# Performance work log

Measured on AMD Instinct MI355X. Metric: run time of the kernel, lower is better.

## Reference

```python
import jax, jax.numpy as jnp
import numpy as np

N = 50000   # nodes
E = 800000  # edges per timestep
T = 2
IN_C = 128
HID = 128


def gcn_conv(x, src, dst, W, b):
    """PyG GCNConv: add self-loops, symmetric normalization, linear, scatter-add, bias."""
    n = x.shape[0]
    loop = jnp.arange(n, dtype=src.dtype)
    s = jnp.concatenate([src, loop])  # [E+N]
    d = jnp.concatenate([dst, loop])
    h = x @ W                          # [N, H]
    deg = jax.ops.segment_sum(jnp.ones_like(d, dtype=x.dtype), d, num_segments=n)
    dinv = jnp.where(deg > 0, jax.lax.rsqrt(deg), 0.0)
    norm = dinv[s] * dinv[d]           # [E+N]
    msg = h[s] * norm[:, None]         # gather + scale
    out = jax.ops.segment_sum(msg, d, num_segments=n)  # scatter-add
    return out + b


def setup_inputs() -> dict:
    key = jax.random.key(0)
    ks = jax.random.split(key, 6)
    x_seq = jax.random.normal(ks[0], (T, N, IN_C), dtype=jnp.float32)
    edge_indices = jax.random.randint(ks[1], (T, 2, E), 0, N, dtype=jnp.int64)
    W1 = jax.random.normal(ks[2], (IN_C, HID), dtype=jnp.float32) * (1.0 / np.sqrt(IN_C))
    b1 = jnp.zeros((HID,), dtype=jnp.float32)
    W2 = jax.random.normal(ks[3], (HID, HID), dtype=jnp.float32) * (1.0 / np.sqrt(HID))
    b2 = jnp.zeros((HID,), dtype=jnp.float32)
    Wc = jax.random.normal(ks[4], (HID, 1), dtype=jnp.float32) * (1.0 / np.sqrt(HID))
    bc = jnp.zeros((1,), dtype=jnp.float32)
    return {"x_seq": x_seq, "edge_indices": edge_indices, "W1": W1, "b1": b1,
            "W2": W2, "b2": b2, "Wc": Wc, "bc": bc}


def reference(x_seq, edge_indices, W1, b1, W2, b2, Wc, bc):
    outputs = []
    for t in range(T):  # small fixed timestep loop, as in original
        x_t = x_seq[t]
        src = edge_indices[t, 0]
        dst = edge_indices[t, 1]
        h = jax.nn.relu(gcn_conv(x_t, src, dst, W1, b1))
        # dropout is inference-identity (eval mode)
        h = gcn_conv(h, src, dst, W2, b2)
        outputs.append(h)
    final = outputs[-1]
    importance_out = (final @ Wc + bc).squeeze(-1)  # [N]
    return (importance_out, *outputs)
```

## Files before the change

kernel.cpp:

```cpp
#include <hip/hip_runtime.h>
#include <hip/hip_bf16.h>

typedef unsigned int u32;
typedef unsigned short u16;
typedef unsigned long long u64;
typedef __bf16 bf16x8 __attribute__((ext_vector_type(8)));
typedef short short8 __attribute__((ext_vector_type(8)));
typedef float floatx4 __attribute__((ext_vector_type(4)));

__device__ inline float b2f(u16 b) { return __uint_as_float((u32)b << 16); }
__device__ inline float lo2f(u32 p) { return __uint_as_float(p << 16); }
__device__ inline float hi2f(u32 p) { return __uint_as_float(p & 0xffff0000u); }
__device__ inline u16 f2bs(float f) {
    __hip_bfloat16 h = __float2bfloat16(f);
    return *reinterpret_cast<u16*>(&h);
}
__device__ inline float ldext(const void* p, int fl, int i) {
    return fl ? ((const float*)p)[i] : b2f(((const u16*)p)[i]);
}

__global__ __launch_bounds__(64) void detect_kernel(const int* __restrict__ eb,
                                                    const u32* __restrict__ xw,
                                                    int* __restrict__ flags,
                                                    int* __restrict__ bkcnt,
                                                    int* __restrict__ ovfcur,
                                                    int S, int n) {
    __shared__ int sh[64 * 3];
    int lane = threadIdx.x & 63;
    for (int j = lane; j < 512; j += 64) bkcnt[j] = 0;
    if (lane == 0) *ovfcur = 0;
    int zc = 0, explo = 0;
#pragma unroll
    for (int r = 0; r < 4; ++r) {
        int i = 64 * r + lane;
        zc += (eb[2 * i + 1] == 0) ? 1 : 0;
        u32 w = xw[i];
        int e = (int)((w >> 7) & 0xFF);
        explo += (e >= 96 && e <= 140) ? 1 : 0;
    }
    sh[lane] = zc;
    sh[64 + lane] = explo;
    __syncthreads();
    int fl = 0;
    {
        int z = 0;
        for (int j = 0; j < 64; ++j) z += sh[j];
        fl = (z > 200) ? 1 : 0;
    }
    int vc = 0;
#pragma unroll
    for (int r = 0; r < 4; ++r) {
        int li = S / 2 + 64 * r + lane;
        int v = fl ? eb[2 * li] : eb[li];
        vc += ((unsigned)v < (unsigned)n) ? 1 : 0;
    }
    sh[128 + lane] = vc;
    __syncthreads();
    if (lane == 0) {
        int vtot = 0, etot = 0;
        for (int j = 0; j < 64; ++j) vtot += sh[128 + j];
        for (int j = 0; j < 64; ++j) etot += sh[64 + j];
        flags[0] = fl;
        flags[1] = (etot >= 192) ? 0 : 1;
        flags[2] = (vtot >= 240) ? (S / 4) : (S / 8);
    }
}

__device__ inline int load_edge(const int* eb, int fl, int idx) {
    return eb[fl ? (idx << 1) : idx];
}

#define PCHUNK 4096
__global__ __launch_bounds__(256) void part_kernel(const int* __restrict__ eb,
                                                   const int* __restrict__ flags,
                                                   int* __restrict__ bkcnt,
                                                   u64* __restrict__ pairs,
                                                   int n, int shift, int capP,
                                                   int gP,
                                                   const void* __restrict__ W1,
                                                   const void* __restrict__ W2,
                                                   u16* __restrict__ W1t,
                                                   u16* __restrict__ W2t) {
    __shared__ int cnt[512];
    __shared__ int gbase[512];
    if ((int)blockIdx.x >= gP) {
        int tid = (blockIdx.x - gP) * 256 + threadIdx.x;
        if (tid < 2 * 128 * 128) {
            int which = tid >> 14;
            int r = tid & 16383;
            const void* W = which ? W2 : W1;
            u16* Wt = which ? W2t : W1t;
            int c = r >> 7, k = r & 127;
            Wt[c * 128 + k] = f2bs(ldext(W, flags[1], k * 128 + c));
        }
        return;
    }
    const int E = flags[2];
    const int fl = flags[0];
    const int nbuk = (2 * n + (1 << shift) - 1) >> shift;
    const int tid = threadIdx.x;
    for (int i = tid; i < nbuk; i += 256) cnt[i] = 0;
    __syncthreads();
    const int e0 = blockIdx.x * PCHUNK;
    u32 sv[16]; int gv[16], rk[16];
#pragma unroll
    for (int j = 0; j < 16; ++j) {
        int e = e0 + j * 256 + tid;
        u32 gs = 0; int g = -1;
        if (e < 2 * E) {
            int t = (e >= E) ? 1 : 0;
            int le = e - t * E;
            gs = (u32)(t * n) + (u32)load_edge(eb, fl, t * 2 * E + le);
            unsigned du = (unsigned)load_edge(eb, fl, t * 2 * E + E + le);
            if (du < (unsigned)n) g = t * n + (int)du;
        }
        sv[j] = gs;
        gv[j] = g;
        rk[j] = (g >= 0) ? atomicAdd(&cnt[g >> shift], 1) : 0;
    }
    __syncthreads();
    for (int b = tid; b < nbuk; b += 256) {
        int c = cnt[b];
        gbase[b] = c ? atomicAdd(&bkcnt[b], c) : 0;
    }
    __syncthreads();
#pragma unroll
    for (int j = 0; j < 16; ++j) {
        if (gv[j] >= 0) {
            int b = gv[j] >> shift;
            int idx = gbase[b] + rk[j];
            if (idx < capP)
                pairs[(size_t)b * capP + idx] =
                    ((u64)(u32)gv[j] << 32) | sv[j];
        }
    }
}

__global__ __launch_bounds__(256) void scat_kernel(const u64* __restrict__ pairs,
                                                   const int* __restrict__ bkcnt,
                                                   int* __restrict__ deg,
                                                   float* __restrict__ dinv,
                                                   int* __restrict__ ssrc,
                                                   int* __restrict__ ovf,
                                                   int* __restrict__ ovfoff,
                                                   int* __restrict__ ovfcur,
                                                   int n2, int shift, int capP) {
    __shared__ int hist[1024];
    __shared__ int cur[1024];
    const int b = blockIdx.x;
    const int d0 = b << shift;
    if (d0 >= n2) return;
    int nn = (1 << shift);
    if (d0 + nn > n2) nn = n2 - d0;
    const int tid = threadIdx.x;
    for (int j = tid; j < nn; j += 256) { hist[j] = 0; cur[j] = 0; }
    __syncthreads();
    int cnt = bkcnt[b];
    if (cnt > capP) cnt = capP;
    const u64* pb = pairs + (size_t)b * capP;
    for (int i = tid; i < cnt; i += 256) {
        unsigned dl = (unsigned)(int)(pb[i] >> 32) - (unsigned)d0;
        if (dl < (unsigned)nn) atomicAdd(&hist[dl], 1);
    }
    __syncthreads();
    for (int j = tid; j < nn; j += 256) {
        int d = hist[j];
        int g = d0 + j;
        deg[g] = d;
        dinv[g] = rsqrtf((float)(d + 1));
        if (d > 32) ovfoff[g] = atomicAdd(ovfcur, d - 32);
    }
    for (int idx = tid; idx < nn * 32; idx += 256) {
        int node = idx >> 5, slot = idx & 31;
        if (slot >= hist[node]) ssrc[(size_t)(d0 + node) * 32 + slot] = n2;
    }
    __syncthreads();
    for (int i = tid; i < cnt; i += 256) {
        u64 p = pb[i];
        unsigned dl = (unsigned)(int)(p >> 32) - (unsigned)d0;
        if (dl < (unsigned)nn) {
            int g = d0 + (int)dl;
            int slot = atomicAdd(&cur[dl], 1);
            u32 v = (u32)p;
            if (v > (u32)n2) v = (u32)n2;
            if (slot < 32) ssrc[(size_t)g * 32 + slot] = (int)v;
            else ovf[ovfoff[g] + slot - 32] = (int)v;
        }
    }
}

__global__ __launch_bounds__(256) void gemm_mfma(const void* __restrict__ Xv,
                                                 int x_ext,
                                                 const u16* __restrict__ Wt,
                                                 const int* __restrict__ flags,
                                                 const float* __restrict__ dinv,
                                                 u16* __restrict__ hs, int n) {
    if (blockIdx.x == 0 && threadIdx.x < 64)
        ((u32*)hs)[(size_t)n * 64 + threadIdx.x] = 0;
    __shared__ u16 Ws[128 * 136];
    {
        u32* wsu = (u32*)Ws;
        const u32* wtu = (const u32*)Wt;
        for (int i = threadIdx.x; i < 128 * 64; i += 256) {
            int c = i >> 6, kk = i & 63;
            wsu[c * 68 + kk] = wtu[i];
        }
    }
    __syncthreads();

    const int wave = threadIdx.x >> 6;
    const int lane = threadIdx.x & 63;
    const int m = lane & 15;
    const int quad = lane >> 4;
    const int node0 = blockIdx.x * 64 + wave * 16;
    if (node0 >= n) return;

    const int xf32 = x_ext ? flags[1] : 0;
    int va = node0 + m;
    if (va > n - 1) va = n - 1;

    floatx4 acc[8];
#pragma unroll
    for (int t = 0; t < 8; ++t) acc[t] = (floatx4){0.f, 0.f, 0.f, 0.f};

#pragma unroll
    for (int ks = 0; ks < 4; ++ks) {
        bf16x8 a;
        if (xf32) {
            const float* Xf = (const float*)Xv + (size_t)va * 128 + ks * 32 + quad * 8;
            float4 x0 = *(const float4*)Xf;
            float4 x1 = *(const float4*)(Xf + 4);
            short8 as;
            as[0] = (short)f2bs(x0.x); as[1] = (short)f2bs(x0.y);
            as[2] = (short)f2bs(x0.z); as[3] = (short)f2bs(x0.w);
            as[4] = (short)f2bs(x1.x); as[5] = (short)f2bs(x1.y);
            as[6] = (short)f2bs(x1.z); as[7] = (short)f2bs(x1.w);
            a = __builtin_bit_cast(bf16x8, as);
        } else {
            const u16* Xb = (const u16*)Xv + (size_t)va * 128 + ks * 32 + quad * 8;
            a = *(const bf16x8*)Xb;
        }
#pragma unroll
        for (int t = 0; t < 8; ++t) {
            const bf16x8 b = *(const bf16x8*)(Ws + (16 * t + m) * 136 + ks * 32 + quad * 8);
            acc[t] = __builtin_amdgcn_mfma_f32_16x16x32_bf16(a, b, acc[t], 0, 0, 0);
        }
    }

#pragma unroll
    for (int r = 0; r < 4; ++r) {
        int v = node0 + quad * 4 + r;
        if (v < n) {
            float dv = dinv[v];
#pragma unroll
            for (int t = 0; t < 8; ++t)
                hs[(size_t)v * 128 + 16 * t + m] = f2bs(acc[t][r] * dv);
        }
    }
}

__global__ __launch_bounds__(256) void gather_kernel(const u16* __restrict__ hs,
                                                     const int* __restrict__ deg,
                                                     const int* __restrict__ ssrc,
                                                     const int* __restrict__ ovf,
                                                     const int* __restrict__ ovfoff,
                                                     const float* __restrict__ dinv,
                                                     const void* __restrict__ bias,
                                                     const int* __restrict__ flags,
                                                     float* __restrict__ outf,
                                                     u16* __restrict__ outb,
                                                     const void* __restrict__ Wc,
                                                     const void* __restrict__ bc,
                                                     float* __restrict__ imp,
                                                     int n2, int half, int relu) {
    const int lane = threadIdx.x & 63;
    int w = __builtin_amdgcn_readfirstlane((blockIdx.x * 256 + threadIdx.x) >> 6);
    if (w >= n2) return;

    const u32* hsu = (const u32*)hs;
    const int dg = __builtin_amdgcn_readfirstlane(deg[w]);
    const int* sp = ssrc + (size_t)w * 32;

    int4 q0 = *(const int4*)(sp);
    int4 q1 = *(const int4*)(sp + 4);
    int4 q2 = *(const int4*)(sp + 8);
    int4 q3 = *(const int4*)(sp + 12);
    u32 pself = hsu[(size_t)w * 64 + lane];

    float ax = lo2f(pself), ay = hi2f(pself);
    float bx = 0.f, by = 0.f, cx = 0.f, cy = 0.f, dx = 0.f, dy = 0.f;

#define ROW(s) hsu[(size_t)(unsigned)(s) * 64 + lane]
    {
        u32 v0 = ROW(q0.x), v1 = ROW(q0.y), v2 = ROW(q0.z), v3 = ROW(q0.w);
        u32 v4 = ROW(q1.x), v5 = ROW(q1.y), v6 = ROW(q1.z), v7 = ROW(q1.w);
        ax += lo2f(v0); ay += hi2f(v0);  bx += lo2f(v1); by += hi2f(v1);
        cx += lo2f(v2); cy += hi2f(v2);  dx += lo2f(v3); dy += hi2f(v3);
        ax += lo2f(v4); ay += hi2f(v4);  bx += lo2f(v5); by += hi2f(v5);
        cx += lo2f(v6); cy += hi2f(v6);  dx += lo2f(v7); dy += hi2f(v7);
    }
    {
        u32 v0 = ROW(q2.x), v1 = ROW(q2.y), v2 = ROW(q2.z), v3 = ROW(q2.w);
        u32 v4 = ROW(q3.x), v5 = ROW(q3.y), v6 = ROW(q3.z), v7 = ROW(q3.w);
        ax += lo2f(v0); ay += hi2f(v0);  bx += lo2f(v1); by += hi2f(v1);
        cx += lo2f(v2); cy += hi2f(v2);  dx += lo2f(v3); dy += hi2f(v3);
        ax += lo2f(v4); ay += hi2f(v4);  bx += lo2f(v5); by += hi2f(v5);
        cx += lo2f(v6); cy += hi2f(v6);  dx += lo2f(v7); dy += hi2f(v7);
    }
    if (dg > 16) {
        int4 q4 = *(const int4*)(sp + 16);
        int4 q5 = *(const int4*)(sp + 20);
        u32 v0 = ROW(q4.x), v1 = ROW(q4.y), v2 = ROW(q4.z), v3 = ROW(q4.w);
        u32 v4 = ROW(q5.x), v5 = ROW(q5.y), v6 = ROW(q5.z), v7 = ROW(q5.w);
        ax += lo2f(v0); ay += hi2f(v0);  bx += lo2f(v1); by += hi2f(v1);
        cx += lo2f(v2); cy += hi2f(v2);  dx += lo2f(v3); dy += hi2f(v3);
        ax += lo2f(v4); ay += hi2f(v4);  bx += lo2f(v5); by += hi2f(v5);
        cx += lo2f(v6); cy += hi2f(v6);  dx += lo2f(v7); dy += hi2f(v7);
    }
    if (dg > 24) {
        int4 q6 = *(const int4*)(sp + 24);
        int4 q7 = *(const int4*)(sp + 28);
        u32 v0 = ROW(q6.x), v1 = ROW(q6.y), v2 = ROW(q6.z), v3 = ROW(q6.w);
        u32 v4 = ROW(q7.x), v5 = ROW(q7.y), v6 = ROW(q7.z), v7 = ROW(q7.w);
        ax += lo2f(v0); ay += hi2f(v0);  bx += lo2f(v1); by += hi2f(v1);
        cx += lo2f(v2); cy += hi2f(v2);  dx += lo2f(v3); dy += hi2f(v3);
        ax += lo2f(v4); ay += hi2f(v4);  bx += lo2f(v5); by += hi2f(v5);
        cx += lo2f(v6); cy += hi2f(v6);  dx += lo2f(v7); dy += hi2f(v7);
    }
    if (dg > 32) {
        int ob = __builtin_amdgcn_readfirstlane(ovfoff[w]);
        int cnt = dg - 32;
        for (int j = 0; j < cnt; ++j) {
            u32 v = ROW(ovf[ob + j]);
            ax += lo2f(v); ay += hi2f(v);
        }
    }
#undef ROW

    ax += bx + cx + dx;
    ay += by + cy + dy;

    const int ffl = flags[1];
    const float dv = dinv[w];
    float o0 = dv * ax + ldext(bias, ffl, 2 * lane);
    float o1 = dv * ay + ldext(bias, ffl, 2 * lane + 1);
    if (relu) {
        o0 = fmaxf(o0, 0.f);
        o1 = fmaxf(o1, 0.f);
    }
    if (outf) ((float2*)outf)[(size_t)w * 64 + lane] = make_float2(o0, o1);
    else ((u32*)outb)[(size_t)w * 64 + lane] = (u32)f2bs(o0) | ((u32)f2bs(o1) << 16);

    if (imp && w >= half) {
        float cb = o0 * ldext(Wc, ffl, 2 * lane) + o1 * ldext(Wc, ffl, 2 * lane + 1);
        cb += __shfl_xor(cb, 32);
        cb += __shfl_xor(cb, 16);
        cb += __shfl_xor(cb, 8);
        cb += __shfl_xor(cb, 4);
        cb += __shfl_xor(cb, 2);
        cb += __shfl_xor(cb, 1);
        if (lane == 0) imp[w - half] = cb + ldext(bc, ffl, 0);
    }
}

extern "C" void kernel_launch(void* const* d_in, const int* in_sizes, int n_in,
                              void* d_out, int out_size, void* d_ws, size_t ws_size,
                              hipStream_t stream) {
    const int T = 2, C = 128;
    const int N = in_sizes[0] / (T * C);
    const int S = in_sizes[1];
    const int Emax = S / 4;
    const int N2 = 2 * N;

    const void* x_seq = d_in[0];
    const int* edges = (const int*)d_in[1];
    const void* W1 = d_in[2];
    const void* b1 = d_in[3];
    const void* W2 = d_in[4];
    const void* b2 = d_in[5];
    const void* Wc = d_in[6];
    const void* bc = d_in[7];

    float* out = (float*)d_out;
    float* R = out + N;

    char* p = (char*)d_ws;
    auto alloc = [&](size_t bytes) {
        char* r = p;
        p += (bytes + 255) & ~(size_t)255;
        return r;
    };
    int* flags = (int*)alloc(256);
    int* deg = (int*)alloc((size_t)N2 * 4);
    float* dinv = (float*)alloc((size_t)N2 * 4);
    int* bkcnt = (int*)alloc(512 * 4);
    int* ovfcur = (int*)alloc(256);
    int* ovfoff = (int*)alloc((size_t)N2 * 4);

    int shift = 8;
    while ((((N2 + (1 << shift) - 1) >> shift) > 512) && shift < 10) ++shift;
    const int NBUK = (N2 + (1 << shift) - 1) >> shift;
    const size_t aliasBytes = (size_t)2 * N2 * C * 2;
    const int capP = (int)(aliasBytes / (8 * (size_t)NBUK)) & ~3;

    int* ssrc = (int*)alloc((size_t)N2 * 32 * 4);
    int* ovf = (int*)alloc((size_t)2 * Emax * 4);
    u16* W1t = (u16*)alloc(128 * 128 * 2);
    u16* W2t = (u16*)alloc(128 * 128 * 2);
    u16* hsb = (u16*)alloc((size_t)(N2 + 2) * C * 2);
    u16* hmb = (u16*)alloc((size_t)N2 * C * 2);
    u64* pairs = (u64*)hsb;

    const int gP = (2 * Emax + PCHUNK - 1) / PCHUNK;
    const int gW = (2 * 128 * 128 + 255) / 256;
    const int gGA = (N2 + 3) / 4;
    const int gG2 = (N2 + 63) / 64;

    detect_kernel<<<1, 64, 0, stream>>>(edges, (const u32*)x_seq, flags, bkcnt,
                                        ovfcur, S, N);

    part_kernel<<<gP + gW, 256, 0, stream>>>(edges, flags, bkcnt, pairs, N, shift,
                                             capP, gP, W1, W2, W1t, W2t);
    scat_kernel<<<NBUK, 256, 0, stream>>>(pairs, bkcnt, deg, dinv, ssrc,
                                          ovf, ovfoff, ovfcur, N2, shift, capP);

    gemm_mfma<<<gG2, 256, 0, stream>>>(x_seq, 1, W1t, flags, dinv, hsb, N2);
    gather_kernel<<<gGA, 256, 0, stream>>>(hsb, deg, ssrc, ovf, ovfoff, dinv, b1,
                                           flags, (float*)nullptr, hmb,
                                           nullptr, nullptr, (float*)nullptr,
                                           N2, N, 1);

    gemm_mfma<<<gG2, 256, 0, stream>>>(hmb, 0, W2t, flags, dinv, hsb, N2);
    gather_kernel<<<gGA, 256, 0, stream>>>(hsb, deg, ssrc, ovf, ovfoff, dinv, b2,
                                           flags, R, (u16*)nullptr,
                                           Wc, bc, out,
                                           N2, N, 0);
}
```

Before: 284.9 us.

## Fuse first GEMM into partition kernel and move dinv scaling into gather

The layer-1 GEMM no longer depends on degree normalization: gather now multiplies each neighbor row by its dinv instead of the GEMM pre-scaling rows. This lets the layer-1 GEMM blocks run inside the edge-partition launch, overlapping dense compute with the edge bucketing and dropping one kernel launch. Weight transposition moves into the detect kernel. Pairs get their own buffer instead of aliasing hsb, which costs extra workspace, and gather adds one scattered dinv load per edge.

Result: no change. 284.4 us (-0.2%).

```diff
diff --git a/kernel.cpp b/kernel.cpp
--- a/kernel.cpp
+++ b/kernel.cpp
@@ -19,82 +19,147 @@
     return fl ? ((const float*)p)[i] : b2f(((const u16*)p)[i]);
 }
 
-__global__ __launch_bounds__(64) void detect_kernel(const int* __restrict__ eb,
-                                                    const u32* __restrict__ xw,
-                                                    int* __restrict__ flags,
-                                                    int* __restrict__ bkcnt,
-                                                    int* __restrict__ ovfcur,
-                                                    int S, int n) {
-    __shared__ int sh[64 * 3];
-    int lane = threadIdx.x & 63;
-    for (int j = lane; j < 512; j += 64) bkcnt[j] = 0;
-    if (lane == 0) *ovfcur = 0;
-    int zc = 0, explo = 0;
-#pragma unroll
-    for (int r = 0; r < 4; ++r) {
-        int i = 64 * r + lane;
-        zc += (eb[2 * i + 1] == 0) ? 1 : 0;
-        u32 w = xw[i];
-        int e = (int)((w >> 7) & 0xFF);
-        explo += (e >= 96 && e <= 140) ? 1 : 0;
-    }
-    sh[lane] = zc;
-    sh[64 + lane] = explo;
-    __syncthreads();
-    int fl = 0;
-    {
-        int z = 0;
-        for (int j = 0; j < 64; ++j) z += sh[j];
-        fl = (z > 200) ? 1 : 0;
-    }
-    int vc = 0;
-#pragma unroll
-    for (int r = 0; r < 4; ++r) {
-        int li = S / 2 + 64 * r + lane;
-        int v = fl ? eb[2 * li] : eb[li];
-        vc += ((unsigned)v < (unsigned)n) ? 1 : 0;
-    }
-    sh[128 + lane] = vc;
-    __syncthreads();
-    if (lane == 0) {
-        int vtot = 0, etot = 0;
-        for (int j = 0; j < 64; ++j) vtot += sh[128 + j];
-        for (int j = 0; j < 64; ++j) etot += sh[64 + j];
-        flags[0] = fl;
-        flags[1] = (etot >= 192) ? 0 : 1;
-        flags[2] = (vtot >= 240) ? (S / 4) : (S / 8);
-    }
-}
-
-__device__ inline int load_edge(const int* eb, int fl, int idx) {
-    return eb[fl ? (idx << 1) : idx];
-}
-
-#define PCHUNK 4096
-__global__ __launch_bounds__(256) void part_kernel(const int* __restrict__ eb,
-                                                   const int* __restrict__ flags,
-                                                   int* __restrict__ bkcnt,
-                                                   u64* __restrict__ pairs,
-                                                   int n, int shift, int capP,
-                                                   int gP,
-                                                   const void* __restrict__ W1,
-                                                   const void* __restrict__ W2,
-                                                   u16* __restrict__ W1t,
-                                                   u16* __restrict__ W2t) {
-    __shared__ int cnt[512];
-    __shared__ int gbase[512];
-    if ((int)blockIdx.x >= gP) {
-        int tid = (blockIdx.x - gP) * 256 + threadIdx.x;
-        if (tid < 2 * 128 * 128) {
-            int which = tid >> 14;
-            int r = tid & 16383;
+__global__ __launch_bounds__(256) void detect_kernel(const int* __restrict__ eb,
+                                                     const u32* __restrict__ xw,
+                                                     int* __restrict__ flags,
+                                                     int* __restrict__ bkcnt,
+                                                     int* __restrict__ ovfcur,
+                                                     float* __restrict__ dinv,
+                                                     const void* __restrict__ W1,
+                                                     const void* __restrict__ W2,
+                                                     u16* __restrict__ W1t,
+                                                     u16* __restrict__ W2t,
+                                                     int S, int n, int n2) {
+    __shared__ int sh[512];
+    __shared__ int res[2];
+    const int tid = threadIdx.x;
+    u32 wx = xw[tid];
+    int e = (int)((wx >> 7) & 0xFF);
+    int explo = (e >= 96 && e <= 140) ? 1 : 0;
+
+    if (blockIdx.x > 0) {
+        sh[tid] = explo;
+        __syncthreads();
+        for (int o = 128; o > 0; o >>= 1) {
+            if (tid < o) sh[tid] += sh[tid + o];
+            __syncthreads();
+        }
+        int fl1 = (sh[0] >= 192) ? 0 : 1;
+        int t2 = ((int)blockIdx.x - 1) * 256 + tid;
+        if (t2 < 2 * 128 * 128) {
+            int which = t2 >> 14, r = t2 & 16383;
             const void* W = which ? W2 : W1;
             u16* Wt = which ? W2t : W1t;
             int c = r >> 7, k = r & 127;
-            Wt[c * 128 + k] = f2bs(ldext(W, flags[1], k * 128 + c));
+            Wt[c * 128 + k] = f2bs(ldext(W, fl1, k * 128 + c));
         }
         return;
     }
+
+    for (int j = tid; j < 512; j += 256) bkcnt[j] = 0;
+    if (tid == 0) { *ovfcur = 0; dinv[n2] = 0.0f; }
+    sh[tid] = (eb[2 * tid + 1] == 0) ? 1 : 0;
+    sh[256 + tid] = explo;
+    __syncthreads();
+    if (tid == 0) {
+        int z = 0, et = 0;
+        for (int j = 0; j < 256; ++j) { z += sh[j]; et += sh[256 + j]; }
+        res[0] = (z > 200) ? 1 : 0;
+        res[1] = et;
+    }
+    __syncthreads();
+    int fl = res[0];
+    int li = S / 2 + tid;
+    int v = fl ? eb[2 * li] : eb[li];
+    sh[tid] = ((unsigned)v < (unsigned)n) ? 1 : 0;
+    __syncthreads();
+    if (tid == 0) {
+        int vt = 0;
+        for (int j = 0; j < 256; ++j) vt += sh[j];
+        flags[0] = fl;
+        flags[1] = (res[1] >= 192) ? 0 : 1;
+        flags[2] = (vt >= 240) ? (S / 4) : (S / 8);
+    }
+}
+
+__device__ inline int load_edge(const int* eb, int fl, int idx) {
+    return eb[fl ? (idx << 1) : idx];
+}
+
+#define PCHUNK 4096
+__global__ __launch_bounds__(256) void part_gemm(const int* __restrict__ eb,
+                                                 const int* __restrict__ flags,
+                                                 int* __restrict__ bkcnt,
+                                                 u64* __restrict__ pairs,
+                                                 int n, int shift, int capP,
+                                                 int gP,
+                                                 const void* __restrict__ Xv,
+                                                 const u16* __restrict__ W1t,
+                                                 u16* __restrict__ hs, int nrows) {
+    __shared__ int cnt[512];
+    __shared__ int gbase[512];
+    __shared__ u16 Ws[128 * 136];
+
+    if ((int)blockIdx.x >= gP) {
+        const int gb = blockIdx.x - gP;
+        if (gb == 0 && threadIdx.x < 64)
+            ((u32*)hs)[(size_t)nrows * 64 + threadIdx.x] = 0;
+        {
+            u32* wsu = (u32*)Ws;
+            const u32* wtu = (const u32*)W1t;
+            for (int i = threadIdx.x; i < 128 * 64; i += 256) {
+                int c = i >> 6, kk = i & 63;
+                wsu[c * 68 + kk] = wtu[i];
+            }
+        }
+        __syncthreads();
+        const int wave = threadIdx.x >> 6;
+        const int lane = threadIdx.x & 63;
+        const int m = lane & 15;
+        const int quad = lane >> 4;
+        const int node0 = gb * 64 + wave * 16;
+        if (node0 >= nrows) return;
+        const int xf32 = flags[1];
+        int va = node0 + m;
+        if (va > nrows - 1) va = nrows - 1;
+        floatx4 acc[8];
+#pragma unroll
+        for (int t = 0; t < 8; ++t) acc[t] = (floatx4){0.f, 0.f, 0.f, 0.f};
+#pragma unroll
+        for (int ks = 0; ks < 4; ++ks) {
+            bf16x8 a;
+            if (xf32) {
+                const float* Xf = (const float*)Xv + (size_t)va * 128 + ks * 32 + quad * 8;
+                float4 x0 = *(const float4*)Xf;
+                float4 x1 = *(const float4*)(Xf + 4);
+                short8 as;
+                as[0] = (short)f2bs(x0.x); as[1] = (short)f2bs(x0.y);
+                as[2] = (short)f2bs(x0.z); as[3] = (short)f2bs(x0.w);
+                as[4] = (short)f2bs(x1.x); as[5] = (short)f2bs(x1.y);
+                as[6] = (short)f2bs(x1.z); as[7] = (short)f2bs(x1.w);
+                a = __builtin_bit_cast(bf16x8, as);
+            } else {
+                const u16* Xb = (const u16*)Xv + (size_t)va * 128 + ks * 32 + quad * 8;
+                a = *(const bf16x8*)Xb;
+            }
+#pragma unroll
+            for (int t = 0; t < 8; ++t) {
+                const bf16x8 b = *(const bf16x8*)(Ws + (16 * t + m) * 136 + ks * 32 + quad * 8);
+                acc[t] = __builtin_amdgcn_mfma_f32_16x16x32_bf16(a, b, acc[t], 0, 0, 0);
+            }
+        }
+#pragma unroll
+        for (int r = 0; r < 4; ++r) {
+            int vv = node0 + quad * 4 + r;
+            if (vv < nrows) {
+#pragma unroll
+                for (int t = 0; t < 8; ++t)
+                    hs[(size_t)vv * 128 + 16 * t + m] = f2bs(acc[t][r]);
+            }
+        }
+        return;
+    }
+
     const int E = flags[2];
     const int fl = flags[0];
     const int nbuk = (2 * n + (1 << shift) - 1) >> shift;
@@ -189,14 +254,11 @@
     }
 }
 
-__global__ __launch_bounds__(256) void gemm_mfma(const void* __restrict__ Xv,
-                                                 int x_ext,
+__global__ __launch_bounds__(256) void gemm_mfma(const u16* __restrict__ Xb0,
                                                  const u16* __restrict__ Wt,
-                                                 const int* __restrict__ flags,
-                                                 const float* __restrict__ dinv,
-                                                 u16* __restrict__ hs, int n) {
+                                                 u16* __restrict__ hs, int nrows) {
     if (blockIdx.x == 0 && threadIdx.x < 64)
-        ((u32*)hs)[(size_t)n * 64 + threadIdx.x] = 0;
+        ((u32*)hs)[(size_t)nrows * 64 + threadIdx.x] = 0;
     __shared__ u16 Ws[128 * 136];
     {
         u32* wsu = (u32*)Ws;
@@ -207,54 +269,34 @@
         }
     }
     __syncthreads();
-
     const int wave = threadIdx.x >> 6;
     const int lane = threadIdx.x & 63;
     const int m = lane & 15;
     const int quad = lane >> 4;
     const int node0 = blockIdx.x * 64 + wave * 16;
-    if (node0 >= n) return;
-
-    const int xf32 = x_ext ? flags[1] : 0;
+    if (node0 >= nrows) return;
     int va = node0 + m;
-    if (va > n - 1) va = n - 1;
-
+    if (va > nrows - 1) va = nrows - 1;
     floatx4 acc[8];
 #pragma unroll
     for (int t = 0; t < 8; ++t) acc[t] = (floatx4){0.f, 0.f, 0.f, 0.f};
-
 #pragma unroll
     for (int ks = 0; ks < 4; ++ks) {
-        bf16x8 a;
-        if (xf32) {
-            const float* Xf = (const float*)Xv + (size_t)va * 128 + ks * 32 + quad * 8;
-            float4 x0 = *(const float4*)Xf;
-            float4 x1 = *(const float4*)(Xf + 4);
-            short8 as;
-            as[0] = (short)f2bs(x0.x); as[1] = (short)f2bs(x0.y);
-            as[2] = (short)f2bs(x0.z); as[3] = (short)f2bs(x0.w);
-            as[4] = (short)f2bs(x1.x); as[5] = (short)f2bs(x1.y);
-            as[6] = (short)f2bs(x1.z); as[7] = (short)f2bs(x1.w);
-            a = __builtin_bit_cast(bf16x8, as);
-        } else {
-            const u16* Xb = (const u16*)Xv + (size_t)va * 128 + ks * 32 + quad * 8;
-            a = *(const bf16x8*)Xb;
-        }
+        const u16* Xb = Xb0 + (size_t)va * 128 + ks * 32 + quad * 8;
+        bf16x8 a = *(const bf16x8*)Xb;
 #pragma unroll
         for (int t = 0; t < 8; ++t) {
             const bf16x8 b = *(const bf16x8*)(Ws + (16 * t + m) * 136 + ks * 32 + quad * 8);
             acc[t] = __builtin_amdgcn_mfma_f32_16x16x32_bf16(a, b, acc[t], 0, 0, 0);
         }
     }
-
 #pragma unroll
     for (int r = 0; r < 4; ++r) {
-        int v = node0 + quad * 4 + r;
-        if (v < n) {
-            float dv = dinv[v];
+        int vv = node0 + quad * 4 + r;
+        if (vv < nrows) {
 #pragma unroll
             for (int t = 0; t < 8; ++t)
-                hs[(size_t)v * 128 + 16 * t + m] = f2bs(acc[t][r] * dv);
+                hs[(size_t)vv * 128 + 16 * t + m] = f2bs(acc[t][r]);
         }
     }
 }
@@ -280,6 +322,7 @@
     const u32* hsu = (const u32*)hs;
     const int dg = __builtin_amdgcn_readfirstlane(deg[w]);
     const int* sp = ssrc + (size_t)w * 32;
+    const float dvw = dinv[w];
 
     int4 q0 = *(const int4*)(sp);
     int4 q1 = *(const int4*)(sp + 4);
@@ -287,63 +330,74 @@
     int4 q3 = *(const int4*)(sp + 12);
     u32 pself = hsu[(size_t)w * 64 + lane];
 
-    float ax = lo2f(pself), ay = hi2f(pself);
+    float ax = dvw * lo2f(pself), ay = dvw * hi2f(pself);
     float bx = 0.f, by = 0.f, cx = 0.f, cy = 0.f, dx = 0.f, dy = 0.f;
 
 #define ROW(s) hsu[(size_t)(unsigned)(s) * 64 + lane]
+#define DV(s) dinv[(unsigned)(s)]
     {
+        float d0 = DV(q0.x), d1 = DV(q0.y), d2 = DV(q0.z), d3 = DV(q0.w);
+        float d4 = DV(q1.x), d5 = DV(q1.y), d6 = DV(q1.z), d7 = DV(q1.w);
         u32 v0 = ROW(q0.x), v1 = ROW(q0.y), v2 = ROW(q0.z), v3 = ROW(q0.w);
         u32 v4 = ROW(q1.x), v5 = ROW(q1.y), v6 = ROW(q1.z), v7 = ROW(q1.w);
-        ax += lo2f(v0); ay += hi2f(v0);  bx += lo2f(v1); by += hi2f(v1);
-        cx += lo2f(v2); cy += hi2f(v2);  dx += lo2f(v3); dy += hi2f(v3);
-        ax += lo2f(v4); ay += hi2f(v4);  bx += lo2f(v5); by += hi2f(v5);
-        cx += lo2f(v6); cy += hi2f(v6);  dx += lo2f(v7); dy += hi2f(v7);
+        ax += d0 * lo2f(v0); ay += d0 * hi2f(v0);  bx += d1 * lo2f(v1); by += d1 * hi2f(v1);
+        cx += d2 * lo2f(v2); cy += d2 * hi2f(v2);  dx += d3 * lo2f(v3); dy += d3 * hi2f(v3);
+        ax += d4 * lo2f(v4); ay += d4 * hi2f(v4);  bx += d5 * lo2f(v5); by += d5 * hi2f(v5);
+        cx += d6 * lo2f(v6); cy += d6 * hi2f(v6);  dx += d7 * lo2f(v7); dy += d7 * hi2f(v7);
     }
     {
+        float d0 = DV(q2.x), d1 = DV(q2.y), d2 = DV(q2.z), d3 = DV(q2.w);
+        float d4 = DV(q3.x), d5 = DV(q3.y), d6 = DV(q3.z), d7 = DV(q3.w);
         u32 v0 = ROW(q2.x), v1 = ROW(q2.y), v2 = ROW(q2.z), v3 = ROW(q2.w);
         u32 v4 = ROW(q3.x), v5 = ROW(q3.y), v6 = ROW(q3.z), v7 = ROW(q3.w);
-        ax += lo2f(v0); ay += hi2f(v0);  bx += lo2f(v1); by += hi2f(v1);
-        cx += lo2f(v2); cy += hi2f(v2);  dx += lo2f(v3); dy += hi2f(v3);
-        ax += lo2f(v4); ay += hi2f(v4);  bx += lo2f(v5); by += hi2f(v5);
-        cx += lo2f(v6); cy += hi2f(v6);  dx += lo2f(v7); dy += hi2f(v7);
+        ax += d0 * lo2f(v0); ay += d0 * hi2f(v0);  bx += d1 * lo2f(v1); by += d1 * hi2f(v1);
+        cx += d2 * lo2f(v2); cy += d2 * hi2f(v2);  dx += d3 * lo2f(v3); dy += d3 * hi2f(v3);
+        ax += d4 * lo2f(v4); ay += d4 * hi2f(v4);  bx += d5 * lo2f(v5); by += d5 * hi2f(v5);
+        cx += d6 * lo2f(v6); cy += d6 * hi2f(v6);  dx += d7 * lo2f(v7); dy += d7 * hi2f(v7);
     }
     if (dg > 16) {
         int4 q4 = *(const int4*)(sp + 16);
         int4 q5 = *(const int4*)(sp + 20);
+        float d0 = DV(q4.x), d1 = DV(q4.y), d2 = DV(q4.z), d3 = DV(q4.w);
+        float d4 = DV(q5.x), d5 = DV(q5.y), d6 = DV(q5.z), d7 = DV(q5.w);
         u32 v0 = ROW(q4.x), v1 = ROW(q4.y), v2 = ROW(q4.z), v3 = ROW(q4.w);
         u32 v4 = ROW(q5.x), v5 = ROW(q5.y), v6 = ROW(q5.z), v7 = ROW(q5.w);
-        ax += lo2f(v0); ay += hi2f(v0);  bx += lo2f(v1); by += hi2f(v1);
-        cx += lo2f(v2); cy += hi2f(v2);  dx += lo2f(v3); dy += hi2f(v3);
-        ax += lo2f(v4); ay += hi2f(v4);  bx += lo2f(v5); by += hi2f(v5);
-        cx += lo2f(v6); cy += hi2f(v6);  dx += lo2f(v7); dy += hi2f(v7);
+        ax += d0 * lo2f(v0); ay += d0 * hi2f(v0);  bx += d1 * lo2f(v1); by += d1 * hi2f(v1);
+        cx += d2 * lo2f(v2); cy += d2 * hi2f(v2);  dx += d3 * lo2f(v3); dy += d3 * hi2f(v3);
+        ax += d4 * lo2f(v4); ay += d4 * hi2f(v4);  bx += d5 * lo2f(v5); by += d5 * hi2f(v5);
+        cx += d6 * lo2f(v6); cy += d6 * hi2f(v6);  dx += d7 * lo2f(v7); dy += d7 * hi2f(v7);
     }
     if (dg > 24) {
         int4 q6 = *(const int4*)(sp + 24);
         int4 q7 = *(const int4*)(sp + 28);
+        float d0 = DV(q6.x), d1 = DV(q6.y), d2 = DV(q6.z), d3 = DV(q6.w);
+        float d4 = DV(q7.x), d5 = DV(q7.y), d6 = DV(q7.z), d7 = DV(q7.w);
         u32 v0 = ROW(q6.x), v1 = ROW(q6.y), v2 = ROW(q6.z), v3 = ROW(q6.w);
         u32 v4 = ROW(q7.x), v5 = ROW(q7.y), v6 = ROW(q7.z), v7 = ROW(q7.w);
-        ax += lo2f(v0); ay += hi2f(v0);  bx += lo2f(v1); by += hi2f(v1);
-        cx += lo2f(v2); cy += hi2f(v2);  dx += lo2f(v3); dy += hi2f(v3);
-        ax += lo2f(v4); ay += hi2f(v4);  bx += lo2f(v5); by += hi2f(v5);
-        cx += lo2f(v6); cy += hi2f(v6);  dx += lo2f(v7); dy += hi2f(v7);
+        ax += d0 * lo2f(v0); ay += d0 * hi2f(v0);  bx += d1 * lo2f(v1); by += d1 * hi2f(v1);
+        cx += d2 * lo2f(v2); cy += d2 * hi2f(v2);  dx += d3 * lo2f(v3); dy += d3 * hi2f(v3);
+        ax += d4 * lo2f(v4); ay += d4 * hi2f(v4);  bx += d5 * lo2f(v5); by += d5 * hi2f(v5);
+        cx += d6 * lo2f(v6); cy += d6 * hi2f(v6);  dx += d7 * lo2f(v7); dy += d7 * hi2f(v7);
     }
     if (dg > 32) {
         int ob = __builtin_amdgcn_readfirstlane(ovfoff[w]);
         int cnt = dg - 32;
         for (int j = 0; j < cnt; ++j) {
-            u32 v = ROW(ovf[ob + j]);
-            ax += lo2f(v); ay += hi2f(v);
+            int s = ovf[ob + j];
+            float dd = DV(s);
+            u32 v = ROW(s);
+            ax += dd * lo2f(v); ay += dd * hi2f(v);
         }
     }
 #undef ROW
+#undef DV
 
     ax += bx + cx + dx;
     ay += by + cy + dy;
 
     const int ffl = flags[1];
-    const float dv = dinv[w];
-    float o0 = dv * ax + ldext(bias, ffl, 2 * lane);
-    float o1 = dv * ay + ldext(bias, ffl, 2 * lane + 1);
+    float o0 = dvw * ax + ldext(bias, ffl, 2 * lane);
+    float o1 = dvw * ay + ldext(bias, ffl, 2 * lane + 1);
     if (relu) {
         o0 = fmaxf(o0, 0.f);
         o1 = fmaxf(o1, 0.f);
@@ -392,7 +446,7 @@
     };
     int* flags = (int*)alloc(256);
     int* deg = (int*)alloc((size_t)N2 * 4);
-    float* dinv = (float*)alloc((size_t)N2 * 4);
+    float* dinv = (float*)alloc((size_t)(N2 + 1) * 4);
     int* bkcnt = (int*)alloc(512 * 4);
     int* ovfcur = (int*)alloc(256);
     int* ovfoff = (int*)alloc((size_t)N2 * 4);
@@ -400,8 +454,8 @@
     int shift = 8;
     while ((((N2 + (1 << shift) - 1) >> shift) > 512) && shift < 10) ++shift;
     const int NBUK = (N2 + (1 << shift) - 1) >> shift;
-    const size_t aliasBytes = (size_t)2 * N2 * C * 2;
-    const int capP = (int)(aliasBytes / (8 * (size_t)NBUK)) & ~3;
+    const size_t pairBytes = (size_t)2 * N2 * C * 2;
+    const int capP = (int)(pairBytes / (8 * (size_t)NBUK)) & ~3;
 
     int* ssrc = (int*)alloc((size_t)N2 * 32 * 4);
     int* ovf = (int*)alloc((size_t)2 * Emax * 4);
@@ -409,28 +463,25 @@
     u16* W2t = (u16*)alloc(128 * 128 * 2);
     u16* hsb = (u16*)alloc((size_t)(N2 + 2) * C * 2);
     u16* hmb = (u16*)alloc((size_t)N2 * C * 2);
-    u64* pairs = (u64*)hsb;
+    u64* pairs = (u64*)alloc((size_t)NBUK * capP * 8);
 
     const int gP = (2 * Emax + PCHUNK - 1) / PCHUNK;
     const int gW = (2 * 128 * 128 + 255) / 256;
     const int gGA = (N2 + 3) / 4;
     const int gG2 = (N2 + 63) / 64;
 
-    detect_kernel<<<1, 64, 0, stream>>>(edges, (const u32*)x_seq, flags, bkcnt,
-                                        ovfcur, S, N);
-
-    part_kernel<<<gP + gW, 256, 0, stream>>>(edges, flags, bkcnt, pairs, N, shift,
-                                             capP, gP, W1, W2, W1t, W2t);
+    detect_kernel<<<1 + gW, 256, 0, stream>>>(edges, (const u32*)x_seq, flags,
+                                              bkcnt, ovfcur, dinv,
+                                              W1, W2, W1t, W2t, S, N, N2);
+    part_gemm<<<gP + gG2, 256, 0, stream>>>(edges, flags, bkcnt, pairs, N, shift,
+                                            capP, gP, x_seq, W1t, hsb, N2);
     scat_kernel<<<NBUK, 256, 0, stream>>>(pairs, bkcnt, deg, dinv, ssrc,
                                           ovf, ovfoff, ovfcur, N2, shift, capP);
-
-    gemm_mfma<<<gG2, 256, 0, stream>>>(x_seq, 1, W1t, flags, dinv, hsb, N2);
     gather_kernel<<<gGA, 256, 0, stream>>>(hsb, deg, ssrc, ovf, ovfoff, dinv, b1,
                                            flags, (float*)nullptr, hmb,
                                            nullptr, nullptr, (float*)nullptr,
                                            N2, N, 1);
-
-    gemm_mfma<<<gG2, 256, 0, stream>>>(hmb, 0, W2t, flags, dinv, hsb, N2);
+    gemm_mfma<<<gG2, 256, 0, stream>>>(hmb, W2t, hsb, N2);
     gather_kernel<<<gGA, 256, 0, stream>>>(hsb, deg, ssrc, ovf, ovfoff, dinv, b2,
                                            flags, R, (u16*)nullptr,
                                            Wc, bc, out,
```
